# Kernel optimization log

Measured on AMD Instinct MI355X. Metric: run time of the kernel, lower is better.

The kernel has to match this reference:

```python
import jax, jax.numpy as jnp
import numpy as np

N_HEADS = 8
N_POINTS = 4


def _bilinear_sample(img, x, y):
    """img: (d, H, W); x, y: (P, H, W) float pixel coords (align_corners=True).
    Zero padding for out-of-bounds (matches F.grid_sample defaults).
    Returns (d, P, H, W)."""
    Hh, Ww = img.shape[1], img.shape[2]
    x0f = jnp.floor(x); y0f = jnp.floor(y)
    x0 = x0f.astype(jnp.int32); x1 = x0 + 1
    y0 = y0f.astype(jnp.int32); y1 = y0 + 1
    wx = x - x0f; wy = y - y0f

    def gather(yi, xi):
        valid = (yi >= 0) & (yi < Hh) & (xi >= 0) & (xi < Ww)
        yc = jnp.clip(yi, 0, Hh - 1)
        xc = jnp.clip(xi, 0, Ww - 1)
        v = img[:, yc, xc]  # (d, P, H, W)
        return v * valid[None].astype(img.dtype)

    out = (gather(y0, x0) * ((1 - wy) * (1 - wx))[None]
           + gather(y0, x1) * ((1 - wy) * wx)[None]
           + gather(y1, x0) * (wy * (1 - wx))[None]
           + gather(y1, x1) * (wy * wx)[None])
    return out


def _forward(query, key, W_off, b_off, W_proj, b_proj):
    B, C, H, W = query.shape
    nh, npts = N_HEADS, N_POINTS
    dh = C // nh
    N = H * W

    # offsets + weights from flattened query tokens
    qf = query.reshape(B, C, N).transpose(0, 2, 1)            # (B, N, C)
    ow = qf @ W_off + b_off                                    # (B, N, nh*npts*3)
    ow = ow.reshape(B, H, W, nh, npts, 3)
    offsets = ow[..., :2]                                      # (B,H,W,nh,npts,2)
    weights = jax.nn.softmax(ow[..., 2], axis=-1)              # (B,H,W,nh,npts)

    # base grid in [-1, 1], (x, y) order
    gy = jnp.linspace(-1.0, 1.0, H, dtype=query.dtype)
    gx = jnp.linspace(-1.0, 1.0, W, dtype=query.dtype)
    gyy, gxx = jnp.meshgrid(gy, gx, indexing='ij')             # (H, W)
    grid = jnp.stack([gxx, gyy], axis=-1)                      # (H, W, 2)

    locs = grid[None, :, :, None, None, :] + offsets * 0.1     # (B,H,W,nh,npts,2)
    locs = locs.transpose(0, 3, 4, 1, 2, 5)                    # (B,nh,npts,H,W,2)
    locs = locs.reshape(B * nh, npts, H, W, 2)

    # normalized -> pixel coords (align_corners=True)
    xpix = (locs[..., 0] + 1.0) * 0.5 * (W - 1)                # (B*nh, npts, H, W)
    ypix = (locs[..., 1] + 1.0) * 0.5 * (H - 1)

    key_r = key.reshape(B * nh, dh, H, W)
    sampled = jax.vmap(_bilinear_sample)(key_r, xpix, ypix)    # (B*nh, dh, npts, H, W)
    sampled = sampled.reshape(B, nh, dh, npts, H, W).transpose(0, 1, 3, 2, 4, 5)  # (B,nh,npts,dh,H,W)

    w = weights.transpose(0, 3, 4, 1, 2)[:, :, :, None, :, :]  # (B,nh,npts,1,H,W)
    out_feat = (sampled * w).sum(axis=2)                       # (B,nh,dh,H,W)
    out_feat = out_feat.reshape(B, C, N).transpose(0, 2, 1)    # (B,N,C)
    return out_feat @ W_proj + b_proj                          # (B,N,C)


def setup_inputs() -> dict:
    key0 = jax.random.key(0)
    ks = jax.random.split(key0, 6)
    B, C, H, W = 8, 256, 64, 64
    query = jax.random.normal(ks[0], (B, C, H, W), dtype=jnp.float32)
    key = jax.random.normal(ks[1], (B, C, H, W), dtype=jnp.float32)
    # small random offset net so sampling deviates from base grid (orig inits to 0)
    W_off = jax.random.normal(ks[2], (C, N_HEADS * N_POINTS * 3), dtype=jnp.float32) * 0.01
    b_off = jax.random.normal(ks[3], (N_HEADS * N_POINTS * 3,), dtype=jnp.float32) * 0.01
    W_proj = jax.random.normal(ks[4], (C, C), dtype=jnp.float32) * (1.0 / np.sqrt(C))
    b_proj = jnp.zeros((C,), dtype=jnp.float32)
    return {"query": query, "key": key, "W_off": W_off, "b_off": b_off,
            "W_proj": W_proj, "b_proj": b_proj}


def reference(query, key, W_off, b_off, W_proj, b_proj):
    return _forward(query, key, W_off, b_off, W_proj, b_proj)
```

## Files before the change

### kernel.cpp

```cpp
#include <hip/hip_runtime.h>

#define NH   8
#define NPTS 4
#define BB   8
#define CCH  256
#define HH   64
#define WW   64
#define NPIX 4096
#define DH   32

__global__ __launch_bounds__(256)
void kA_offsets(const float* __restrict__ query, const float* __restrict__ W_off,
                const float* __restrict__ b_off, float4* __restrict__ coords)
{
    __shared__ float w_lds[64][96];

    const int t  = threadIdx.x;
    const int g0 = blockIdx.x * 64;
    const int b  = g0 >> 12;
    const int n0 = g0 & (NPIX - 1);

    const int px = t & 63;
    const int jg = t >> 6;
    const int j0 = jg * 24;

    const float* qcol = query + (size_t)b * CCH * NPIX + n0 + px;

    float acc[24];
#pragma unroll
    for (int i = 0; i < 24; ++i) acc[i] = 0.f;

    for (int kc = 0; kc < CCH; kc += 64) {
#pragma unroll
        for (int ii = 0; ii < 6; ++ii) {
            int i4 = t + ii * 256;
            int k  = i4 / 24;
            int j4 = i4 - k * 24;
            *(float4*)&w_lds[k][j4 << 2] =
                *(const float4*)(W_off + (size_t)(kc + k) * 96 + (j4 << 2));
        }
        __syncthreads();
#pragma unroll 8
        for (int k = 0; k < 64; ++k) {
            float a = qcol[(size_t)(kc + k) * NPIX];
#pragma unroll
            for (int j4 = 0; j4 < 6; ++j4) {
                float4 w = *(const float4*)&w_lds[k][j0 + (j4 << 2)];
                acc[j4 * 4 + 0] = fmaf(a, w.x, acc[j4 * 4 + 0]);
                acc[j4 * 4 + 1] = fmaf(a, w.y, acc[j4 * 4 + 1]);
                acc[j4 * 4 + 2] = fmaf(a, w.z, acc[j4 * 4 + 2]);
                acc[j4 * 4 + 3] = fmaf(a, w.w, acc[j4 * 4 + 3]);
            }
        }
        __syncthreads();
    }

    const int n = n0 + px;
    const int x = n & 63;
    const int y = n >> 6;
    const float fx = (float)x, fy = (float)y;

#pragma unroll
    for (int hh = 0; hh < 2; ++hh) {
        const int head = jg * 2 + hh;
        const int lb   = hh * 12;
        float ox[4], oy[4], l[4];
#pragma unroll
        for (int p = 0; p < 4; ++p) {
            ox[p] = acc[lb + p * 3 + 0] + b_off[j0 + lb + p * 3 + 0];
            oy[p] = acc[lb + p * 3 + 1] + b_off[j0 + lb + p * 3 + 1];
            l[p]  = acc[lb + p * 3 + 2] + b_off[j0 + lb + p * 3 + 2];
        }
        float m = fmaxf(fmaxf(l[0], l[1]), fmaxf(l[2], l[3]));
        float e[4], s = 0.f;
#pragma unroll
        for (int p = 0; p < 4; ++p) { e[p] = __expf(l[p] - m); s += e[p]; }
        float inv = 1.f / s;
        float4* cp = coords + ((size_t)(b * NPIX + n) * NH + head) * NPTS;
#pragma unroll
        for (int p = 0; p < 4; ++p) {
            cp[p] = make_float4(fx + ox[p] * 3.15f, fy + oy[p] * 3.15f, e[p] * inv, 0.f);
        }
    }
}

__global__ __launch_bounds__(256)
void kT_transpose(const float* __restrict__ key, float* __restrict__ keyT)
{
    __shared__ float tile[64][65];
    int bid = blockIdx.x;
    const int nt = bid & 63; bid >>= 6;
    const int ct = bid & 3;  bid >>= 2;
    const int b  = bid;
    const int n0 = nt * 64, c0 = ct * 64;
    const int t = threadIdx.x;

    const float* src = key + ((size_t)b * CCH + c0) * NPIX + n0;
#pragma unroll
    for (int ii = 0; ii < 4; ++ii) {
        int idx = t + ii * 256;
        int cc = idx >> 4, q = idx & 15;
        float4 v = *(const float4*)(src + (size_t)cc * NPIX + (q << 2));
        tile[cc][(q << 2) + 0] = v.x;
        tile[cc][(q << 2) + 1] = v.y;
        tile[cc][(q << 2) + 2] = v.z;
        tile[cc][(q << 2) + 3] = v.w;
    }
    __syncthreads();
    float* dst = keyT + ((size_t)(b * NPIX + n0)) * CCH + c0;
#pragma unroll
    for (int ii = 0; ii < 4; ++ii) {
        int idx = t + ii * 256;
        int nn = idx >> 4, q = idx & 15;
        float4 v = make_float4(tile[(q << 2) + 0][nn], tile[(q << 2) + 1][nn],
                               tile[(q << 2) + 2][nn], tile[(q << 2) + 3][nn]);
        *(float4*)(dst + (size_t)nn * CCH + (q << 2)) = v;
    }
}

__global__ __launch_bounds__(256)
void kB_gather(const float* __restrict__ keyT, const float4* __restrict__ coords,
               float* __restrict__ feat)
{
    const int bid  = blockIdx.x;
    const int sbid = (bid & 7) * 1024 + (bid >> 3);

    const int t  = threadIdx.x;
    const int wv = t >> 6, l = t & 63;
    const int g  = sbid * 4 + wv;
    const int b  = g >> 12;
    const int head = l >> 3;
    const int cl   = (l & 7) << 2;
    const int c    = head * DH + cl;

    const float*  kb = keyT + (((size_t)b << 12)) * CCH;
    const float4* cp = coords + ((size_t)g * NH + head) * NPTS;

    float4 acc = make_float4(0.f, 0.f, 0.f, 0.f);
#pragma unroll
    for (int pt = 0; pt < 4; ++pt) {
        float4 co = cp[pt];
        float xp = co.x, yp = co.y, wgt = co.z;
        float x0f = floorf(xp), y0f = floorf(yp);
        int   x0  = (int)x0f,  y0  = (int)y0f;
        float wx  = xp - x0f,  wy  = yp - y0f;
#pragma unroll
        for (int cr = 0; cr < 4; ++cr) {
            int   xi = x0 + (cr & 1);
            int   yi = y0 + (cr >> 1);
            float wc = ((cr & 1) ? wx : 1.f - wx) * ((cr >> 1) ? wy : 1.f - wy);
            bool  valid = (xi >= 0) && (xi < WW) && (yi >= 0) && (yi < HH);
            int   xc = min(max(xi, 0), WW - 1);
            int   yc = min(max(yi, 0), HH - 1);
            float ww = valid ? (wgt * wc) : 0.f;
            float4 v = *(const float4*)(kb + ((size_t)((yc << 6) + xc)) * CCH + c);
            acc.x = fmaf(ww, v.x, acc.x);
            acc.y = fmaf(ww, v.y, acc.y);
            acc.z = fmaf(ww, v.z, acc.z);
            acc.w = fmaf(ww, v.w, acc.w);
        }
    }
    *(float4*)(feat + (size_t)g * CCH + c) = acc;
}

__global__ __launch_bounds__(256)
void kB_sample(const float* __restrict__ key, const float4* __restrict__ coords,
               float* __restrict__ feat)
{
    __shared__ float cx[4][64], cy[4][64], cw[4][64];

    const int t = threadIdx.x;
    int bi = blockIdx.x;
    const int y    = bi & 63; bi >>= 6;
    const int head = bi & 7;  bi >>= 3;
    const int b    = bi;

    {
        const int xx = t >> 2, pt = t & 3;
        float4 v = coords[((size_t)(b * NPIX + y * WW + xx) * NH + head) * NPTS + pt];
        cx[pt][xx] = v.x; cy[pt][xx] = v.y; cw[pt][xx] = v.z;
    }
    __syncthreads();

    const int x  = t & 63;
    const int cg = t >> 6;
    const int c0 = head * DH + cg * 8;
    const float* kbase = key + ((size_t)b * CCH + c0) * NPIX;

    float acc[8];
#pragma unroll
    for (int i = 0; i < 8; ++i) acc[i] = 0.f;

#pragma unroll
    for (int pt = 0; pt < 4; ++pt) {
        float xp = cx[pt][x], yp = cy[pt][x], wgt = cw[pt][x];
        float x0f = floorf(xp), y0f = floorf(yp);
        int   x0  = (int)x0f,  y0  = (int)y0f;
        float wx  = xp - x0f,  wy  = yp - y0f;
#pragma unroll
        for (int cr = 0; cr < 4; ++cr) {
            int   xi = x0 + (cr & 1);
            int   yi = y0 + (cr >> 1);
            float wc = ((cr & 1) ? wx : 1.f - wx) * ((cr >> 1) ? wy : 1.f - wy);
            bool  valid = (xi >= 0) && (xi < WW) && (yi >= 0) && (yi < HH);
            int   xc = min(max(xi, 0), WW - 1);
            int   yc = min(max(yi, 0), HH - 1);
            const float* p = kbase + yc * WW + xc;
            float ww = valid ? (wgt * wc) : 0.f;
#pragma unroll
            for (int c = 0; c < 8; ++c)
                acc[c] = fmaf(ww, p[(size_t)c * NPIX], acc[c]);
        }
    }

    float* fp = feat + (size_t)(b * NPIX + y * WW + x) * CCH + c0;
    *(float4*)fp       = make_float4(acc[0], acc[1], acc[2], acc[3]);
    *(float4*)(fp + 4) = make_float4(acc[4], acc[5], acc[6], acc[7]);
}

__global__ __launch_bounds__(256)
void kC_proj(const float* __restrict__ feat, const float* __restrict__ W_proj,
             const float* __restrict__ b_proj, float* __restrict__ out)
{
    __shared__ float a_lds[32][132];
    __shared__ float b_lds[32][128];

    const int t  = threadIdx.x;
    const int mb = blockIdx.x >> 1;
    const int nb = blockIdx.x & 1;
    const int m0 = mb * 128, n0 = nb * 128;

    const int tm = t >> 4, tn = t & 15;
    const int ra = t >> 3, qa = t & 7;
    const int kb = t >> 5, qb = t & 31;

    float acc[8][8];
#pragma unroll
    for (int i = 0; i < 8; ++i)
#pragma unroll
        for (int j = 0; j < 8; ++j) acc[i][j] = 0.f;

    for (int kc = 0; kc < 256; kc += 32) {
        float4 a[4];
#pragma unroll
        for (int ii = 0; ii < 4; ++ii)
            a[ii] = *(const float4*)(feat + (size_t)(m0 + ra + ii * 32) * 256 + kc + (qa << 2));
        float4 w[4];
#pragma unroll
        for (int ii = 0; ii < 4; ++ii)
            w[ii] = *(const float4*)(W_proj + (size_t)(kc + kb + ii * 8) * 256 + n0 + (qb << 2));
        __syncthreads();
#pragma unroll
        for (int ii = 0; ii < 4; ++ii) {
            const int r = ra + ii * 32;
            a_lds[(qa << 2) + 0][r] = a[ii].x;
            a_lds[(qa << 2) + 1][r] = a[ii].y;
            a_lds[(qa << 2) + 2][r] = a[ii].z;
            a_lds[(qa << 2) + 3][r] = a[ii].w;
        }
#pragma unroll
        for (int ii = 0; ii < 4; ++ii)
            *(float4*)&b_lds[kb + ii * 8][qb << 2] = w[ii];
        __syncthreads();
#pragma unroll
        for (int k = 0; k < 32; ++k) {
            float4 av0 = *(const float4*)&a_lds[k][tm << 2];
            float4 av1 = *(const float4*)&a_lds[k][64 + (tm << 2)];
            float4 bv0 = *(const float4*)&b_lds[k][tn << 2];
            float4 bv1 = *(const float4*)&b_lds[k][64 + (tn << 2)];
            float ar[8] = {av0.x, av0.y, av0.z, av0.w, av1.x, av1.y, av1.z, av1.w};
            float br[8] = {bv0.x, bv0.y, bv0.z, bv0.w, bv1.x, bv1.y, bv1.z, bv1.w};
#pragma unroll
            for (int i = 0; i < 8; ++i)
#pragma unroll
                for (int j = 0; j < 8; ++j)
                    acc[i][j] = fmaf(ar[i], br[j], acc[i][j]);
        }
    }

    const float4 bp0 = *(const float4*)(b_proj + n0 + (tn << 2));
    const float4 bp1 = *(const float4*)(b_proj + n0 + 64 + (tn << 2));
    const float bpr[8] = {bp0.x, bp0.y, bp0.z, bp0.w, bp1.x, bp1.y, bp1.z, bp1.w};
#pragma unroll
    for (int i = 0; i < 8; ++i) {
        const int m = m0 + ((i < 4) ? 0 : 64) + (tm << 2) + (i & 3);
        float* op = out + (size_t)m * 256 + n0;
        *(float4*)(op + (tn << 2)) =
            make_float4(acc[i][0] + bpr[0], acc[i][1] + bpr[1],
                        acc[i][2] + bpr[2], acc[i][3] + bpr[3]);
        *(float4*)(op + 64 + (tn << 2)) =
            make_float4(acc[i][4] + bpr[4], acc[i][5] + bpr[5],
                        acc[i][6] + bpr[6], acc[i][7] + bpr[7]);
    }
}

extern "C" void kernel_launch(void* const* d_in, const int* in_sizes, int n_in,
                              void* d_out, int out_size, void* d_ws, size_t ws_size,
                              hipStream_t stream)
{
    const float* query  = (const float*)d_in[0];
    const float* key    = (const float*)d_in[1];
    const float* W_off  = (const float*)d_in[2];
    const float* b_off  = (const float*)d_in[3];
    const float* W_proj = (const float*)d_in[4];
    const float* b_proj = (const float*)d_in[5];
    float* out = (float*)d_out;

    const size_t keyT_bytes   = (size_t)BB * NPIX * CCH * sizeof(float);
    const size_t coords_bytes = (size_t)BB * NPIX * NH * NPTS * sizeof(float4);
    const size_t feat_bytes   = (size_t)BB * NPIX * CCH * sizeof(float);

    if (ws_size >= keyT_bytes + coords_bytes + feat_bytes) {
        float*  keyT   = (float*)d_ws;
        float4* coords = (float4*)((char*)d_ws + keyT_bytes);
        float*  feat   = (float*)((char*)d_ws + keyT_bytes + coords_bytes);

        kA_offsets<<<(BB * NPIX) / 64, 256, 0, stream>>>(query, W_off, b_off, coords);
        kT_transpose<<<BB * 4 * 64, 256, 0, stream>>>(key, keyT);
        kB_gather<<<(BB * NPIX) / 4, 256, 0, stream>>>(keyT, coords, feat);
        kC_proj<<<(BB * NPIX / 128) * 2, 256, 0, stream>>>(feat, W_proj, b_proj, out);
    } else {
        float4* coords = (float4*)d_ws;
        float*  feat   = (float*)((char*)d_ws + coords_bytes);

        kA_offsets<<<(BB * NPIX) / 64, 256, 0, stream>>>(query, W_off, b_off, coords);
        kB_sample<<<BB * NH * HH, 256, 0, stream>>>(key, coords, feat);
        kC_proj<<<(BB * NPIX / 128) * 2, 256, 0, stream>>>(feat, W_proj, b_proj, out);
    }
}
```

Baseline: 277.7 us.

## Register-tile offset GEMM with LDS-staged query and 4x12 per-thread blocking

```diff
diff --git a/kernel.cpp b/kernel.cpp
--- a/kernel.cpp
+++ b/kernel.cpp
@@ -10,77 +10,101 @@
 #define DH   32
 
 __global__ __launch_bounds__(256)
-void kA_offsets(const float* __restrict__ query, const float* __restrict__ W_off,
-                const float* __restrict__ b_off, float4* __restrict__ coords)
-{
-    __shared__ float w_lds[64][96];
+void kA_gemm(const float* __restrict__ query, const float* __restrict__ W_off,
+             const float* __restrict__ b_off, float4* __restrict__ coords)
+{
+    __shared__ float a_lds[64][128];
+    __shared__ float w_lds[64][100];
 
     const int t  = threadIdx.x;
-    const int g0 = blockIdx.x * 64;
-    const int b  = g0 >> 12;
-    const int n0 = g0 & (NPIX - 1);
-
-    const int px = t & 63;
-    const int jg = t >> 6;
-    const int j0 = jg * 24;
-
-    const float* qcol = query + (size_t)b * CCH * NPIX + n0 + px;
-
-    float acc[24];
-#pragma unroll
-    for (int i = 0; i < 24; ++i) acc[i] = 0.f;
+    const int m0 = blockIdx.x * 128;
+    const int b  = m0 >> 12;
+    const int n0 = m0 & (NPIX - 1);
+    const float* qbase = query + (size_t)b * CCH * NPIX + n0;
+
+    const int tm = t >> 3;
+    const int tj = t & 7;
+
+    float acc[4][12];
+#pragma unroll
+    for (int i = 0; i < 4; ++i)
+#pragma unroll
+        for (int j = 0; j < 12; ++j) acc[i][j] = 0.f;
 
     for (int kc = 0; kc < CCH; kc += 64) {
+        float4 a[8];
+#pragma unroll
+        for (int ii = 0; ii < 8; ++ii) {
+            const int idx = t + ii * 256;
+            a[ii] = *(const float4*)(qbase + (size_t)(kc + (idx >> 5)) * NPIX
+                                     + ((idx & 31) << 2));
+        }
+        float4 w[6];
 #pragma unroll
         for (int ii = 0; ii < 6; ++ii) {
-            int i4 = t + ii * 256;
-            int k  = i4 / 24;
-            int j4 = i4 - k * 24;
-            *(float4*)&w_lds[k][j4 << 2] =
-                *(const float4*)(W_off + (size_t)(kc + k) * 96 + (j4 << 2));
+            const int idx = t + ii * 256;
+            const int kk = idx / 24, q = idx - kk * 24;
+            w[ii] = *(const float4*)(W_off + (size_t)(kc + kk) * 96 + (q << 2));
         }
         __syncthreads();
-#pragma unroll 8
+#pragma unroll
+        for (int ii = 0; ii < 8; ++ii) {
+            const int idx = t + ii * 256;
+            *(float4*)&a_lds[idx >> 5][(idx & 31) << 2] = a[ii];
+        }
+#pragma unroll
+        for (int ii = 0; ii < 6; ++ii) {
+            const int idx = t + ii * 256;
+            const int kk = idx / 24, q = idx - kk * 24;
+            *(float4*)&w_lds[kk][q << 2] = w[ii];
+        }
+        __syncthreads();
+#pragma unroll 16
         for (int k = 0; k < 64; ++k) {
-            float a = qcol[(size_t)(kc + k) * NPIX];
-#pragma unroll
-            for (int j4 = 0; j4 < 6; ++j4) {
-                float4 w = *(const float4*)&w_lds[k][j0 + (j4 << 2)];
-                acc[j4 * 4 + 0] = fmaf(a, w.x, acc[j4 * 4 + 0]);
-                acc[j4 * 4 + 1] = fmaf(a, w.y, acc[j4 * 4 + 1]);
-                acc[j4 * 4 + 2] = fmaf(a, w.z, acc[j4 * 4 + 2]);
-                acc[j4 * 4 + 3] = fmaf(a, w.w, acc[j4 * 4 + 3]);
-            }
-        }
-        __syncthreads();
-    }
-
-    const int n = n0 + px;
-    const int x = n & 63;
-    const int y = n >> 6;
-    const float fx = (float)x, fy = (float)y;
-
-#pragma unroll
-    for (int hh = 0; hh < 2; ++hh) {
-        const int head = jg * 2 + hh;
-        const int lb   = hh * 12;
+            const float4 av = *(const float4*)&a_lds[k][tm << 2];
+            const float4 w0 = *(const float4*)&w_lds[k][tj * 12];
+            const float4 w1 = *(const float4*)&w_lds[k][tj * 12 + 4];
+            const float4 w2 = *(const float4*)&w_lds[k][tj * 12 + 8];
+            const float ar[4] = {av.x, av.y, av.z, av.w};
+            const float wr[12] = {w0.x, w0.y, w0.z, w0.w,
+                                  w1.x, w1.y, w1.z, w1.w,
+                                  w2.x, w2.y, w2.z, w2.w};
+#pragma unroll
+            for (int i = 0; i < 4; ++i)
+#pragma unroll
+                for (int j = 0; j < 12; ++j)
+                    acc[i][j] = fmaf(ar[i], wr[j], acc[i][j]);
+        }
+    }
+
+    float bo[12];
+#pragma unroll
+    for (int j = 0; j < 12; ++j) bo[j] = b_off[tj * 12 + j];
+
+#pragma unroll
+    for (int i = 0; i < 4; ++i) {
+        const int g = m0 + (tm << 2) + i;
+        const int n = g & (NPIX - 1);
+        const float fx = (float)(n & 63), fy = (float)(n >> 6);
+
         float ox[4], oy[4], l[4];
 #pragma unroll
         for (int p = 0; p < 4; ++p) {
-            ox[p] = acc[lb + p * 3 + 0] + b_off[j0 + lb + p * 3 + 0];
-            oy[p] = acc[lb + p * 3 + 1] + b_off[j0 + lb + p * 3 + 1];
-            l[p]  = acc[lb + p * 3 + 2] + b_off[j0 + lb + p * 3 + 2];
+            ox[p] = acc[i][p * 3 + 0] + bo[p * 3 + 0];
+            oy[p] = acc[i][p * 3 + 1] + bo[p * 3 + 1];
+            l[p]  = acc[i][p * 3 + 2] + bo[p * 3 + 2];
         }
         float m = fmaxf(fmaxf(l[0], l[1]), fmaxf(l[2], l[3]));
         float e[4], s = 0.f;
 #pragma unroll
         for (int p = 0; p < 4; ++p) { e[p] = __expf(l[p] - m); s += e[p]; }
-        float inv = 1.f / s;
-        float4* cp = coords + ((size_t)(b * NPIX + n) * NH + head) * NPTS;
-#pragma unroll
-        for (int p = 0; p < 4; ++p) {
-            cp[p] = make_float4(fx + ox[p] * 3.15f, fy + oy[p] * 3.15f, e[p] * inv, 0.f);
-        }
+        const float inv = 1.f / s;
+
+        float4* cp = coords + ((size_t)g * NH + tj) * NPTS;
+#pragma unroll
+        for (int p = 0; p < 4; ++p)
+            cp[p] = make_float4(fx + ox[p] * 3.15f, fy + oy[p] * 3.15f,
+                                e[p] * inv, 0.f);
     }
 }
 
@@ -315,7 +339,7 @@
         float4* coords = (float4*)((char*)d_ws + keyT_bytes);
         float*  feat   = (float*)((char*)d_ws + keyT_bytes + coords_bytes);
 
-        kA_offsets<<<(BB * NPIX) / 64, 256, 0, stream>>>(query, W_off, b_off, coords);
+        kA_gemm<<<(BB * NPIX) / 128, 256, 0, stream>>>(query, W_off, b_off, coords);
         kT_transpose<<<BB * 4 * 64, 256, 0, stream>>>(key, keyT);
         kB_gather<<<(BB * NPIX) / 4, 256, 0, stream>>>(keyT, coords, feat);
         kC_proj<<<(BB * NPIX / 128) * 2, 256, 0, stream>>>(feat, W_proj, b_proj, out);
@@ -323,7 +347,7 @@
         float4* coords = (float4*)d_ws;
         float*  feat   = (float*)((char*)d_ws + coords_bytes);
 
-        kA_offsets<<<(BB * NPIX) / 64, 256, 0, stream>>>(query, W_off, b_off, coords);
+        kA_gemm<<<(BB * NPIX) / 128, 256, 0, stream>>>(query, W_off, b_off, coords);
         kB_sample<<<BB * NH * HH, 256, 0, stream>>>(key, coords, feat);
         kC_proj<<<(BB * NPIX / 128) * 2, 256, 0, stream>>>(feat, W_proj, b_proj, out);
     }
```

Result: faster. 246.8 us (-11.1%).
